# Kernel optimization log

Measured on AMD Instinct MI355X. Metric: run time of the kernel, lower is better.

The kernel has to match this reference:

```python
import jax, jax.numpy as jnp
import numpy as np

B, D_IN, D_HID, D_OUT = 32768, 512, 1024, 2048

def setup_inputs() -> dict:
    key = jax.random.key(0)
    k1, k2, k3, k4 = jax.random.split(key, 4)
    x = jax.random.normal(k1, (B, D_IN), dtype=jnp.float32)
    # linear1 params (torch Linear default-style init, scale approximated)
    l1_w = jax.random.normal(k2, (D_HID, D_IN), dtype=jnp.float32) * (D_IN ** -0.5)
    l1_b = jax.random.normal(k3, (D_HID,), dtype=jnp.float32) * 0.01
    # second linear params: normal(0, hidden^-0.5) weight, zero bias as in source
    weight = jax.random.normal(k4, (D_OUT, D_HID), dtype=jnp.float32) * (D_HID ** -0.5)
    bias = jnp.zeros((D_OUT,), dtype=jnp.float32)
    return {"x": x, "l1_w": l1_w, "l1_b": l1_b, "weight": weight, "bias": bias}

def reference(x, l1_w, l1_b, weight, bias):
    # linear1: [B, D_IN] -> [B, D_HID]
    h = jnp.einsum('bi,hi->bh', x, l1_w) + l1_b
    # fused linear + max epilogue: scores [B, D_OUT] -> max over output dim
    scores = jnp.einsum('bh,oh->bo', h, weight) + bias
    return jnp.max(scores, axis=-1)  # [B]
```

## Files before the change

kernel.cpp:

```cpp
#include <hip/hip_runtime.h>
#include <hip/hip_bf16.h>
#include <stdint.h>

static constexpr int BATCH = 32768;
static constexpr int DIN   = 512;
static constexpr int DHID  = 1024;
static constexpr int DOUT  = 2048;

typedef __bf16 bf16x8 __attribute__((ext_vector_type(8)));
typedef float  f32x4  __attribute__((ext_vector_type(4)));

__device__ __forceinline__ unsigned short f2bf(float f) {
    unsigned int u = __float_as_uint(f);
    u += 0x7FFFu + ((u >> 16) & 1u);
    return (unsigned short)(u >> 16);
}

__device__ __forceinline__ void gload_lds16(const void* g, void* l) {
    __builtin_amdgcn_global_load_lds((__attribute__((address_space(1))) void*)g,
                                     (__attribute__((address_space(3))) void*)l,
                                     16, 0, 0);
}


__global__ __launch_bounds__(256) void prep_kernel(
    const float* __restrict__ w1, const float4* __restrict__ w2f,
    const float4* __restrict__ xf, const float* __restrict__ b1,
    const float* __restrict__ b2,
    unsigned short* __restrict__ w1t, ushort4* __restrict__ w2b,
    ushort4* __restrict__ xb, float* __restrict__ bp) {
    const int blk = blockIdx.x;
    const int t   = threadIdx.x;
    if (blk < 512) {
        __shared__ float tile[32][33];
        const int tileI = blk & 15;
        const int tileH = blk >> 4;
        const int iBase = tileI * 32, hBase = tileH * 32;
        const int col = t & 31, rowq = t >> 5;
#pragma unroll
        for (int p = 0; p < 4; ++p) {
            const int row = p * 8 + rowq;
            tile[row][col] = w1[(size_t)(hBase + row) * DIN + iBase + col];
        }
        __syncthreads();
#pragma unroll
        for (int p = 0; p < 4; ++p) {
            const int row = p * 8 + rowq;
            w1t[(size_t)(iBase + row) * DHID + hBase + col] = f2bf(tile[col][row]);
        }
    } else if (blk < 2560) {
        __shared__ float wsum[4];
        const int o = blk - 512;
        const size_t g = (size_t)o * 256 + t;
        float4 v = w2f[g];
        ushort4 ob;
        ob.x = f2bf(v.x); ob.y = f2bf(v.y); ob.z = f2bf(v.z); ob.w = f2bf(v.w);
        w2b[g] = ob;
        float4 bv = ((const float4*)b1)[t];
        float s = v.x * bv.x + v.y * bv.y + v.z * bv.z + v.w * bv.w;
#pragma unroll
        for (int off = 1; off < 64; off <<= 1) s += __shfl_xor(s, off);
        if ((t & 63) == 0) wsum[t >> 6] = s;
        __syncthreads();
        if (t == 0) bp[o] = wsum[0] + wsum[1] + wsum[2] + wsum[3] + b2[o];
    } else {
        const size_t g = (size_t)(blk - 2560) * 256 + t;
        float4 v = xf[g];
        ushort4 o;
        o.x = f2bf(v.x); o.y = f2bf(v.y); o.z = f2bf(v.z); o.w = f2bf(v.w);
        xb[g] = o;
    }
}

__global__ __launch_bounds__(256) void gemmW_kernel(
    const unsigned short* __restrict__ A,
    const unsigned short* __restrict__ Bw,
    unsigned short* __restrict__ W) {
    constexpr int K = DHID;
    __shared__ __align__(16) unsigned short sA[64 * 128];
    __shared__ __align__(16) unsigned short sB[64 * 128];

    const int tid  = threadIdx.x;
    const int lane = tid & 63;
    const int wid  = tid >> 6;
    const int wr = wid >> 1, wc = wid & 1;
    const int r = lane & 15, q = lane >> 4;
    const int blockN = blockIdx.x * 64;
    const int blockM = blockIdx.y * 64;

    const int chKey = (tid & 15) ^ ((tid >> 4) & 15);
    const size_t aBase = (size_t)(blockM + (tid >> 4)) * K + chKey * 8;
    const size_t bBase = (size_t)(blockN + (tid >> 4)) * K + chKey * 8;

    f32x4 acc[2][2];
#pragma unroll
    for (int mt = 0; mt < 2; ++mt)
#pragma unroll
        for (int nt = 0; nt < 2; ++nt) { f32x4 z = {0.f, 0.f, 0.f, 0.f}; acc[mt][nt] = z; }

    for (int k0 = 0; k0 < K; k0 += 128) {
#pragma unroll
        for (int j = 0; j < 4; ++j) {
            gload_lds16(A  + aBase + (size_t)j * 16 * K + k0, sA + j * 2048 + wid * 512);
            gload_lds16(Bw + bBase + (size_t)j * 16 * K + k0, sB + j * 2048 + wid * 512);
        }
        __syncthreads();
#pragma unroll
        for (int ks = 0; ks < 4; ++ks) {
            const int ch = ((ks << 2) + q) ^ r;
            bf16x8 af[2], bf[2];
#pragma unroll
            for (int mt = 0; mt < 2; ++mt) af[mt] = *(const bf16x8*)&sA[(wr * 32 + mt * 16 + r) * 128 + ch * 8];
#pragma unroll
            for (int nt = 0; nt < 2; ++nt) bf[nt] = *(const bf16x8*)&sB[(wc * 32 + nt * 16 + r) * 128 + ch * 8];
#pragma unroll
            for (int mt = 0; mt < 2; ++mt)
#pragma unroll
                for (int nt = 0; nt < 2; ++nt)
                    acc[mt][nt] = __builtin_amdgcn_mfma_f32_16x16x32_bf16(af[mt], bf[nt], acc[mt][nt], 0, 0, 0);
        }
        __syncthreads();
    }

#pragma unroll
    for (int mt = 0; mt < 2; ++mt) {
        const int row0 = blockM + wr * 32 + mt * 16 + q * 4;
#pragma unroll
        for (int nt = 0; nt < 2; ++nt) {
            const int col = blockN + wc * 32 + nt * 16 + r;
#pragma unroll
            for (int reg = 0; reg < 4; ++reg)
                W[(size_t)(row0 + reg) * DIN + col] = f2bf(acc[mt][nt][reg]);
        }
    }
}

__global__ __launch_bounds__(512, 2) void gemmS_kernel(
    const unsigned short* __restrict__ A,
    const unsigned short* __restrict__ Bw,
    const float* __restrict__ bp,
    float* __restrict__ partials) {
    constexpr int K = DIN;
    __shared__ __align__(16) unsigned short lds[65536];

    const int tid  = threadIdx.x;
    const int lane = tid & 63;
    const int wid  = tid >> 6;
    const int wr   = wid >> 2;
    const int wc   = wid & 3;
    const int r    = lane & 15, q = lane >> 4;

    const int g    = blockIdx.x;
    const int xcd  = g & 7;
    const int i    = g >> 3;
    const int mIdx = xcd * 16 + (i >> 3);
    const int nIdx = i & 7;
    const int blockM = mIdx * 256;
    const int blockN = nIdx * 256;

    const int sRow = tid >> 2;
    const int swz  = (tid & 3) ^ ((tid >> 3) & 3);
    const unsigned short* aSrc = A  + (size_t)(blockM + sRow) * K + swz * 8;
    const unsigned short* bSrc = Bw + (size_t)(blockN + sRow) * K + swz * 8;
    unsigned short* ldsW = lds + wid * 512;

#define STAGE(srcPtr, isB, buf, kh, kt) do {                                    \
    gload_lds16((srcPtr) + (kt) * 64 + (kh) * 32,                               \
                ldsW + (buf) * 32768 + (isB) * 16384 + (kh) * 8192);            \
    gload_lds16((srcPtr) + 128 * K + (kt) * 64 + (kh) * 32,                     \
                ldsW + (buf) * 32768 + (isB) * 16384 + (kh) * 8192 + 4096);     \
} while (0)

    const int rsw  = (r >> 1) & 3;
    const int fOff = (q ^ rsw) * 8;
    const unsigned short* ldsAf = lds + (wr * 128 + r) * 32 + fOff;
    const unsigned short* ldsBf = lds + 16384 + (wc * 64 + r) * 32 + fOff;

    f32x4 acc[8][4];
#pragma unroll
    for (int mt = 0; mt < 8; ++mt)
#pragma unroll
        for (int nt = 0; nt < 4; ++nt) { f32x4 z = {0.f, 0.f, 0.f, 0.f}; acc[mt][nt] = z; }
    bf16x8 af[4], bfr[4];

#define LDA(buf, ks, mg) do {                                                   \
    const unsigned short* p_ = ldsAf + (buf) * 32768 + (ks) * 8192 + (mg) * 2048; \
    af[0] = *(const bf16x8*)(p_);                                               \
    af[1] = *(const bf16x8*)(p_ + 512);                                         \
    af[2] = *(const bf16x8*)(p_ + 1024);                                        \
    af[3] = *(const bf16x8*)(p_ + 1536);                                        \
} while (0)
#define LDB(buf, ks) do {                                                       \
    const unsigned short* p_ = ldsBf + (buf) * 32768 + (ks) * 8192;             \
    bfr[0] = *(const bf16x8*)(p_);                                              \
    bfr[1] = *(const bf16x8*)(p_ + 512);                                        \
    bfr[2] = *(const bf16x8*)(p_ + 1024);                                       \
    bfr[3] = *(const bf16x8*)(p_ + 1536);                                       \
} while (0)
#define MM(mg) do {                                                             \
    __builtin_amdgcn_s_setprio(1);                                              \
    _Pragma("unroll") for (int m_ = 0; m_ < 4; ++m_)                            \
    _Pragma("unroll") for (int n_ = 0; n_ < 4; ++n_)                            \
        acc[(mg) * 4 + m_][n_] = __builtin_amdgcn_mfma_f32_16x16x32_bf16(       \
            af[m_], bfr[n_], acc[(mg) * 4 + m_][n_], 0, 0, 0);                  \
    __builtin_amdgcn_s_setprio(0);                                              \
} while (0)
#define BAR()   __builtin_amdgcn_s_barrier()
#define LGKM0() asm volatile("s_waitcnt lgkmcnt(0)" ::: "memory")
#define VMC(n)  asm volatile("s_waitcnt vmcnt(" #n ")" ::: "memory")

    STAGE(bSrc, 1, 0, 0, 0);
    STAGE(aSrc, 0, 0, 0, 0);
    STAGE(bSrc, 1, 0, 1, 0);
    STAGE(aSrc, 0, 0, 1, 0);
    STAGE(bSrc, 1, 1, 0, 1);
    STAGE(aSrc, 0, 1, 0, 1);
    STAGE(bSrc, 1, 1, 1, 1);
    VMC(6);
    BAR();

#pragma unroll 1
    for (int it = 0; it < 3; ++it) {
        const int t1 = 2 * it + 1, n0 = 2 * it + 2, n1 = 2 * it + 3;
        LDA(0, 0, 0); LDB(0, 0); STAGE(aSrc, 0, 1, 1, t1);
        BAR(); LGKM0(); MM(0); BAR();
        LDA(0, 0, 1); STAGE(bSrc, 1, 0, 0, n0);
        BAR(); LGKM0(); MM(1); BAR();
        LDA(0, 1, 0); LDB(0, 1); STAGE(aSrc, 0, 0, 0, n0);
        BAR(); LGKM0(); MM(0); BAR();
        LDA(0, 1, 1); STAGE(bSrc, 1, 0, 1, n0); VMC(6);
        BAR(); LGKM0(); MM(1); BAR();
        LDA(1, 0, 0); LDB(1, 0); STAGE(aSrc, 0, 0, 1, n0);
        BAR(); LGKM0(); MM(0); BAR();
        LDA(1, 0, 1); STAGE(bSrc, 1, 1, 0, n1);
        BAR(); LGKM0(); MM(1); BAR();
        LDA(1, 1, 0); LDB(1, 1); STAGE(aSrc, 0, 1, 0, n1);
        BAR(); LGKM0(); MM(0); BAR();
        LDA(1, 1, 1); STAGE(bSrc, 1, 1, 1, n1); VMC(6);
        BAR(); LGKM0(); MM(1); BAR();
    }
    LDA(0, 0, 0); LDB(0, 0); STAGE(aSrc, 0, 1, 1, 7);
    BAR(); LGKM0(); MM(0); BAR();
    LDA(0, 0, 1);
    BAR(); LGKM0(); MM(1); BAR();
    LDA(0, 1, 0); LDB(0, 1);
    BAR(); LGKM0(); MM(0); BAR();
    LDA(0, 1, 1); VMC(0);
    BAR(); LGKM0(); MM(1); BAR();
    LDA(1, 0, 0); LDB(1, 0);
    BAR(); LGKM0(); MM(0); BAR();
    LDA(1, 0, 1);
    BAR(); LGKM0(); MM(1); BAR();
    LDA(1, 1, 0); LDB(1, 1);
    BAR(); LGKM0(); MM(0); BAR();
    LDA(1, 1, 1);
    BAR(); LGKM0(); MM(1);

#undef STAGE
#undef LDA
#undef LDB
#undef MM
#undef BAR
#undef LGKM0
#undef VMC

    const int colBase = blockN + wc * 64;
    float bv[4];
#pragma unroll
    for (int nt = 0; nt < 4; ++nt) bv[nt] = bp[colBase + nt * 16 + r];

#pragma unroll
    for (int mt = 0; mt < 8; ++mt) {
#pragma unroll
        for (int reg = 0; reg < 4; ++reg) {
            float v = fmaxf(fmaxf(acc[mt][0][reg] + bv[0], acc[mt][1][reg] + bv[1]),
                            fmaxf(acc[mt][2][reg] + bv[2], acc[mt][3][reg] + bv[3]));
#pragma unroll
            for (int off = 1; off < 16; off <<= 1)
                v = fmaxf(v, __shfl_xor(v, off));
            if (r == 0) {
                const int row = blockM + wr * 128 + mt * 16 + q * 4 + reg;
                partials[(size_t)row * 32 + nIdx * 4 + wc] = v;
            }
        }
    }
}

__global__ __launch_bounds__(256) void reduce_kernel(
    const float4* __restrict__ partials, float* __restrict__ out) {
    const int row = blockIdx.x * blockDim.x + threadIdx.x;
    const float4* p = partials + (size_t)row * 8;
    float m = -INFINITY;
#pragma unroll
    for (int i = 0; i < 8; ++i) {
        float4 v = p[i];
        m = fmaxf(m, fmaxf(fmaxf(v.x, v.y), fmaxf(v.z, v.w)));
    }
    out[row] = m;
}

extern "C" void kernel_launch(void* const* d_in, const int* in_sizes, int n_in,
                              void* d_out, int out_size, void* d_ws, size_t ws_size,
                              hipStream_t stream) {
    const float* x   = (const float*)d_in[0];
    const float* l1w = (const float*)d_in[1];
    const float* l1b = (const float*)d_in[2];
    const float* w2  = (const float*)d_in[3];
    const float* b2  = (const float*)d_in[4];
    float* out = (float*)d_out;

    char* ws = (char*)d_ws;
    unsigned short* w1t = (unsigned short*)(ws);
    unsigned short* w2b = (unsigned short*)(ws + 1048576);
    unsigned short* Wb  = (unsigned short*)(ws + 5242880);
    float* bp           = (float*)(ws + 7340032);
    unsigned short* xb  = (unsigned short*)(ws + 7348224);
    float* partials     = (float*)(ws + 40902656);

    prep_kernel<<<18944, 256, 0, stream>>>(
        l1w, (const float4*)w2, (const float4*)x, l1b, b2,
        w1t, (ushort4*)w2b, (ushort4*)xb, bp);

    gemmW_kernel<<<dim3(DIN / 64, DOUT / 64), 256, 0, stream>>>(w2b, w1t, Wb);

    gemmS_kernel<<<1024, 512, 0, stream>>>(xb, Wb, bp, partials);

    reduce_kernel<<<BATCH / 256, 256, 0, stream>>>((const float4*)partials, out);
}
```

Measured before the change: 192.7 us.

## Make gemmS persistent over four M tiles, prefetching next tile during K tail

The score GEMM now launches 256 blocks instead of 1024. Each block walks four consecutive 256-row M tiles for a fixed N tile. The next tile's first A/B K-slices are staged into LDS during the current tile's last K steps, which removes the per-block prologue and drain bubbles. The B tile stays hot across tiles. In exchange there are fewer blocks than two per CU on a 256-CU part, and the epilogue max-reduction now runs serially between tiles, where it can stall the pipeline.

```diff
diff --git a/kernel.cpp b/kernel.cpp
--- a/kernel.cpp
+++ b/kernel.cpp
@@ -150,18 +150,18 @@
     const int wc   = wid & 3;
     const int r    = lane & 15, q = lane >> 4;
 
-    const int g    = blockIdx.x;
-    const int xcd  = g & 7;
-    const int i    = g >> 3;
-    const int mIdx = xcd * 16 + (i >> 3);
-    const int nIdx = i & 7;
-    const int blockM = mIdx * 256;
-    const int blockN = nIdx * 256;
+    const int b    = blockIdx.x;
+    const int xcd  = b & 7;
+    const int j    = b >> 3;
+    const int nIdx = j & 7;
+    const int mGrp = xcd * 4 + (j >> 3);
+    const int blockM0 = mGrp * 4 * 256;
+    const int blockN  = nIdx * 256;
 
     const int sRow = tid >> 2;
     const int swz  = (tid & 3) ^ ((tid >> 3) & 3);
-    const unsigned short* aSrc = A  + (size_t)(blockM + sRow) * K + swz * 8;
-    const unsigned short* bSrc = Bw + (size_t)(blockN + sRow) * K + swz * 8;
+    const unsigned short* aCur = A  + (size_t)(blockM0 + sRow) * K + swz * 8;
+    const unsigned short* bSrc = Bw + (size_t)(blockN  + sRow) * K + swz * 8;
     unsigned short* ldsW = lds + wid * 512;
 
 #define STAGE(srcPtr, isB, buf, kh, kt) do {                                    \
@@ -209,52 +209,110 @@
 #define LGKM0() asm volatile("s_waitcnt lgkmcnt(0)" ::: "memory")
 #define VMC(n)  asm volatile("s_waitcnt vmcnt(" #n ")" ::: "memory")
 
+#define EPILOG(tt) do {                                                         \
+    const int rowB_ = blockM0 + (tt) * 256 + wr * 128;                          \
+    _Pragma("unroll") for (int mt_ = 0; mt_ < 8; ++mt_) {                       \
+        _Pragma("unroll") for (int rg_ = 0; rg_ < 4; ++rg_) {                   \
+            float v_ = fmaxf(fmaxf(acc[mt_][0][rg_] + bv[0],                    \
+                                   acc[mt_][1][rg_] + bv[1]),                   \
+                             fmaxf(acc[mt_][2][rg_] + bv[2],                    \
+                                   acc[mt_][3][rg_] + bv[3]));                  \
+            _Pragma("unroll") for (int of_ = 1; of_ < 16; of_ <<= 1)            \
+                v_ = fmaxf(v_, __shfl_xor(v_, of_));                            \
+            if (r == 0) {                                                       \
+                const int row_ = rowB_ + mt_ * 16 + q * 4 + rg_;                \
+                partials[(size_t)row_ * 32 + nIdx * 4 + wc] = v_;               \
+            }                                                                   \
+        }                                                                       \
+    }                                                                           \
+} while (0)
+
+#define ACC_ZERO() do {                                                         \
+    _Pragma("unroll") for (int mt_ = 0; mt_ < 8; ++mt_)                         \
+    _Pragma("unroll") for (int nt_ = 0; nt_ < 4; ++nt_) {                       \
+        f32x4 z_ = {0.f, 0.f, 0.f, 0.f}; acc[mt_][nt_] = z_;                    \
+    }                                                                           \
+} while (0)
+
+    const int colBase = blockN + wc * 64;
+    float bv[4];
+#pragma unroll
+    for (int nt = 0; nt < 4; ++nt) bv[nt] = bp[colBase + nt * 16 + r];
+    VMC(0);
+
     STAGE(bSrc, 1, 0, 0, 0);
-    STAGE(aSrc, 0, 0, 0, 0);
+    STAGE(aCur, 0, 0, 0, 0);
     STAGE(bSrc, 1, 0, 1, 0);
-    STAGE(aSrc, 0, 0, 1, 0);
+    STAGE(aCur, 0, 0, 1, 0);
     STAGE(bSrc, 1, 1, 0, 1);
-    STAGE(aSrc, 0, 1, 0, 1);
+    STAGE(aCur, 0, 1, 0, 1);
     STAGE(bSrc, 1, 1, 1, 1);
     VMC(6);
     BAR();
 
 #pragma unroll 1
-    for (int it = 0; it < 3; ++it) {
-        const int t1 = 2 * it + 1, n0 = 2 * it + 2, n1 = 2 * it + 3;
-        LDA(0, 0, 0); LDB(0, 0); STAGE(aSrc, 0, 1, 1, t1);
-        BAR(); LGKM0(); MM(0); BAR();
-        LDA(0, 0, 1); STAGE(bSrc, 1, 0, 0, n0);
-        BAR(); LGKM0(); MM(1); BAR();
-        LDA(0, 1, 0); LDB(0, 1); STAGE(aSrc, 0, 0, 0, n0);
-        BAR(); LGKM0(); MM(0); BAR();
-        LDA(0, 1, 1); STAGE(bSrc, 1, 0, 1, n0); VMC(6);
-        BAR(); LGKM0(); MM(1); BAR();
-        LDA(1, 0, 0); LDB(1, 0); STAGE(aSrc, 0, 0, 1, n0);
-        BAR(); LGKM0(); MM(0); BAR();
-        LDA(1, 0, 1); STAGE(bSrc, 1, 1, 0, n1);
-        BAR(); LGKM0(); MM(1); BAR();
-        LDA(1, 1, 0); LDB(1, 1); STAGE(aSrc, 0, 1, 0, n1);
-        BAR(); LGKM0(); MM(0); BAR();
-        LDA(1, 1, 1); STAGE(bSrc, 1, 1, 1, n1); VMC(6);
-        BAR(); LGKM0(); MM(1); BAR();
-    }
-    LDA(0, 0, 0); LDB(0, 0); STAGE(aSrc, 0, 1, 1, 7);
-    BAR(); LGKM0(); MM(0); BAR();
-    LDA(0, 0, 1);
-    BAR(); LGKM0(); MM(1); BAR();
-    LDA(0, 1, 0); LDB(0, 1);
-    BAR(); LGKM0(); MM(0); BAR();
-    LDA(0, 1, 1); VMC(0);
-    BAR(); LGKM0(); MM(1); BAR();
-    LDA(1, 0, 0); LDB(1, 0);
-    BAR(); LGKM0(); MM(0); BAR();
-    LDA(1, 0, 1);
-    BAR(); LGKM0(); MM(1); BAR();
-    LDA(1, 1, 0); LDB(1, 1);
-    BAR(); LGKM0(); MM(0); BAR();
-    LDA(1, 1, 1);
-    BAR(); LGKM0(); MM(1);
+    for (int t = 0; t < 4; ++t) {
+#pragma unroll 1
+        for (int i2 = 0; i2 < 3; ++i2) {
+            const int k1 = 2 * i2 + 1, k2 = 2 * i2 + 2, k3 = 2 * i2 + 3;
+            LDA(0, 0, 0); LDB(0, 0); STAGE(aCur, 0, 1, 1, k1);
+            BAR(); LGKM0(); MM(0); BAR();
+            LDA(0, 0, 1); STAGE(bSrc, 1, 0, 0, k2);
+            BAR(); LGKM0(); MM(1); BAR();
+            LDA(0, 1, 0); LDB(0, 1); STAGE(aCur, 0, 0, 0, k2);
+            BAR(); LGKM0(); MM(0); BAR();
+            LDA(0, 1, 1); STAGE(bSrc, 1, 0, 1, k2); VMC(6);
+            BAR(); LGKM0(); MM(1); BAR();
+            LDA(1, 0, 0); LDB(1, 0); STAGE(aCur, 0, 0, 1, k2);
+            BAR(); LGKM0(); MM(0); BAR();
+            LDA(1, 0, 1); STAGE(bSrc, 1, 1, 0, k3);
+            BAR(); LGKM0(); MM(1); BAR();
+            LDA(1, 1, 0); LDB(1, 1); STAGE(aCur, 0, 1, 0, k3);
+            BAR(); LGKM0(); MM(0); BAR();
+            LDA(1, 1, 1); STAGE(bSrc, 1, 1, 1, k3); VMC(6);
+            BAR(); LGKM0(); MM(1); BAR();
+        }
+        if (t < 3) {
+            const unsigned short* aNxt = aCur + 256 * K;
+            LDA(0, 0, 0); LDB(0, 0); STAGE(aCur, 0, 1, 1, 7);
+            BAR(); LGKM0(); MM(0); BAR();
+            LDA(0, 0, 1); STAGE(bSrc, 1, 0, 0, 0);
+            BAR(); LGKM0(); MM(1); BAR();
+            LDA(0, 1, 0); LDB(0, 1); STAGE(aNxt, 0, 0, 0, 0);
+            BAR(); LGKM0(); MM(0); BAR();
+            LDA(0, 1, 1); STAGE(bSrc, 1, 0, 1, 0); VMC(6);
+            BAR(); LGKM0(); MM(1); BAR();
+            LDA(1, 0, 0); LDB(1, 0); STAGE(aNxt, 0, 0, 1, 0);
+            BAR(); LGKM0(); MM(0); BAR();
+            LDA(1, 0, 1); STAGE(bSrc, 1, 1, 0, 1);
+            BAR(); LGKM0(); MM(1); BAR();
+            LDA(1, 1, 0); LDB(1, 1); STAGE(aNxt, 0, 1, 0, 1);
+            BAR(); LGKM0(); MM(0); BAR();
+            LDA(1, 1, 1); STAGE(bSrc, 1, 1, 1, 1); VMC(6);
+            BAR(); LGKM0(); MM(1); BAR();
+            EPILOG(t);
+            ACC_ZERO();
+            aCur = aNxt;
+        } else {
+            LDA(0, 0, 0); LDB(0, 0); STAGE(aCur, 0, 1, 1, 7);
+            BAR(); LGKM0(); MM(0); BAR();
+            LDA(0, 0, 1);
+            BAR(); LGKM0(); MM(1); BAR();
+            LDA(0, 1, 0); LDB(0, 1);
+            BAR(); LGKM0(); MM(0); BAR();
+            LDA(0, 1, 1); VMC(0);
+            BAR(); LGKM0(); MM(1); BAR();
+            LDA(1, 0, 0); LDB(1, 0);
+            BAR(); LGKM0(); MM(0); BAR();
+            LDA(1, 0, 1);
+            BAR(); LGKM0(); MM(1); BAR();
+            LDA(1, 1, 0); LDB(1, 1);
+            BAR(); LGKM0(); MM(0); BAR();
+            LDA(1, 1, 1);
+            BAR(); LGKM0(); MM(1);
+            EPILOG(3);
+        }
+    }
 
 #undef STAGE
 #undef LDA
@@ -263,27 +321,8 @@
 #undef BAR
 #undef LGKM0
 #undef VMC
-
-    const int colBase = blockN + wc * 64;
-    float bv[4];
-#pragma unroll
-    for (int nt = 0; nt < 4; ++nt) bv[nt] = bp[colBase + nt * 16 + r];
-
-#pragma unroll
-    for (int mt = 0; mt < 8; ++mt) {
-#pragma unroll
-        for (int reg = 0; reg < 4; ++reg) {
-            float v = fmaxf(fmaxf(acc[mt][0][reg] + bv[0], acc[mt][1][reg] + bv[1]),
-                            fmaxf(acc[mt][2][reg] + bv[2], acc[mt][3][reg] + bv[3]));
-#pragma unroll
-            for (int off = 1; off < 16; off <<= 1)
-                v = fmaxf(v, __shfl_xor(v, off));
-            if (r == 0) {
-                const int row = blockM + wr * 128 + mt * 16 + q * 4 + reg;
-                partials[(size_t)row * 32 + nIdx * 4 + wc] = v;
-            }
-        }
-    }
+#undef EPILOG
+#undef ACC_ZERO
 }
 
 __global__ __launch_bounds__(256) void reduce_kernel(
@@ -323,7 +362,7 @@
 
     gemmW_kernel<<<dim3(DIN / 64, DOUT / 64), 256, 0, stream>>>(w2b, w1t, Wb);
 
-    gemmS_kernel<<<1024, 512, 0, stream>>>(xb, Wb, bp, partials);
+    gemmS_kernel<<<256, 512, 0, stream>>>(xb, Wb, bp, partials);
 
     reduce_kernel<<<BATCH / 256, 256, 0, stream>>>((const float4*)partials, out);
 }
```

Result: slower. 357.3 us (+85.4%).

## Loop each gemmS block over four N tiles with running max accumulation

Applied to the files above, without the earlier changes.

The scores GEMM now launches 256 blocks instead of 1024. Each block owns one 256-row M tile and walks four consecutive 256-column N tiles, prefetching the next B tile during the tail of the current one. After each tile it folds the bias-added accumulators into a per-thread running max held in registers, then zeroes them. This cuts the partials footprint fourfold and simplifies the reduce kernel, but 256 blocks may underfill the GPU's CUs and the extra mx registers may raise register pressure.

```diff
diff --git a/kernel.cpp b/kernel.cpp
--- a/kernel.cpp
+++ b/kernel.cpp
@@ -141,7 +141,7 @@
     const float* __restrict__ bp,
     float* __restrict__ partials) {
     constexpr int K = DIN;
-    __shared__ __align__(16) unsigned short lds[65536];
+    __shared__ __align__(16) unsigned short lds[67584];
 
     const int tid  = threadIdx.x;
     const int lane = tid & 63;
@@ -150,19 +150,20 @@
     const int wc   = wid & 3;
     const int r    = lane & 15, q = lane >> 4;
 
-    const int g    = blockIdx.x;
-    const int xcd  = g & 7;
-    const int i    = g >> 3;
-    const int mIdx = xcd * 16 + (i >> 3);
-    const int nIdx = i & 7;
-    const int blockM = mIdx * 256;
-    const int blockN = nIdx * 256;
+    const int b    = blockIdx.x;
+    const int xcd  = b & 7;
+    const int j    = b >> 3;
+    const int nGrp = j & 1;
+    const int mIdx = xcd * 16 + (j >> 1);
+    const int blockM  = mIdx * 256;
+    const int blockN0 = nGrp * 1024;
 
     const int sRow = tid >> 2;
     const int swz  = (tid & 3) ^ ((tid >> 3) & 3);
-    const unsigned short* aSrc = A  + (size_t)(blockM + sRow) * K + swz * 8;
-    const unsigned short* bSrc = Bw + (size_t)(blockN + sRow) * K + swz * 8;
+    const unsigned short* aSrc = A  + (size_t)(blockM  + sRow) * K + swz * 8;
+    const unsigned short* bCur = Bw + (size_t)(blockN0 + sRow) * K + swz * 8;
     unsigned short* ldsW = lds + wid * 512;
+    float* biasLds = (float*)(lds + 65536);
 
 #define STAGE(srcPtr, isB, buf, kh, kt) do {                                    \
     gload_lds16((srcPtr) + (kt) * 64 + (kh) * 32,                               \
@@ -181,7 +182,13 @@
     for (int mt = 0; mt < 8; ++mt)
 #pragma unroll
         for (int nt = 0; nt < 4; ++nt) { f32x4 z = {0.f, 0.f, 0.f, 0.f}; acc[mt][nt] = z; }
+    float mx[8][4];
+#pragma unroll
+    for (int mt = 0; mt < 8; ++mt)
+#pragma unroll
+        for (int rg = 0; rg < 4; ++rg) mx[mt][rg] = -INFINITY;
     bf16x8 af[4], bfr[4];
+    float bvc[4];
 
 #define LDA(buf, ks, mg) do {                                                   \
     const unsigned short* p_ = ldsAf + (buf) * 32768 + (ks) * 8192 + (mg) * 2048; \
@@ -209,52 +216,109 @@
 #define LGKM0() asm volatile("s_waitcnt lgkmcnt(0)" ::: "memory")
 #define VMC(n)  asm volatile("s_waitcnt vmcnt(" #n ")" ::: "memory")
 
-    STAGE(bSrc, 1, 0, 0, 0);
+#define FOLD() do {                                                             \
+    _Pragma("unroll") for (int mt_ = 0; mt_ < 8; ++mt_)                         \
+    _Pragma("unroll") for (int rg_ = 0; rg_ < 4; ++rg_) {                       \
+        float v_ = fmaxf(fmaxf(acc[mt_][0][rg_] + bvc[0],                       \
+                               acc[mt_][1][rg_] + bvc[1]),                      \
+                         fmaxf(acc[mt_][2][rg_] + bvc[2],                       \
+                               acc[mt_][3][rg_] + bvc[3]));                     \
+        mx[mt_][rg_] = fmaxf(mx[mt_][rg_], v_);                                 \
+    }                                                                           \
+} while (0)
+
+#define ACC_ZERO() do {                                                         \
+    _Pragma("unroll") for (int mt_ = 0; mt_ < 8; ++mt_)                         \
+    _Pragma("unroll") for (int nt_ = 0; nt_ < 4; ++nt_) {                       \
+        f32x4 z_ = {0.f, 0.f, 0.f, 0.f}; acc[mt_][nt_] = z_;                    \
+    }                                                                           \
+} while (0)
+
+    {
+        float2 bb = ((const float2*)(bp + blockN0))[tid];
+        ((float2*)biasLds)[tid] = bb;
+    }
+    LGKM0();
+
+    STAGE(bCur, 1, 0, 0, 0);
     STAGE(aSrc, 0, 0, 0, 0);
-    STAGE(bSrc, 1, 0, 1, 0);
+    STAGE(bCur, 1, 0, 1, 0);
     STAGE(aSrc, 0, 0, 1, 0);
-    STAGE(bSrc, 1, 1, 0, 1);
+    STAGE(bCur, 1, 1, 0, 1);
     STAGE(aSrc, 0, 1, 0, 1);
-    STAGE(bSrc, 1, 1, 1, 1);
+    STAGE(bCur, 1, 1, 1, 1);
     VMC(6);
     BAR();
 
+#pragma unroll
+    for (int nt = 0; nt < 4; ++nt) bvc[nt] = biasLds[wc * 64 + nt * 16 + r];
+
 #pragma unroll 1
-    for (int it = 0; it < 3; ++it) {
-        const int t1 = 2 * it + 1, n0 = 2 * it + 2, n1 = 2 * it + 3;
-        LDA(0, 0, 0); LDB(0, 0); STAGE(aSrc, 0, 1, 1, t1);
-        BAR(); LGKM0(); MM(0); BAR();
-        LDA(0, 0, 1); STAGE(bSrc, 1, 0, 0, n0);
-        BAR(); LGKM0(); MM(1); BAR();
-        LDA(0, 1, 0); LDB(0, 1); STAGE(aSrc, 0, 0, 0, n0);
-        BAR(); LGKM0(); MM(0); BAR();
-        LDA(0, 1, 1); STAGE(bSrc, 1, 0, 1, n0); VMC(6);
-        BAR(); LGKM0(); MM(1); BAR();
-        LDA(1, 0, 0); LDB(1, 0); STAGE(aSrc, 0, 0, 1, n0);
-        BAR(); LGKM0(); MM(0); BAR();
-        LDA(1, 0, 1); STAGE(bSrc, 1, 1, 0, n1);
-        BAR(); LGKM0(); MM(1); BAR();
-        LDA(1, 1, 0); LDB(1, 1); STAGE(aSrc, 0, 1, 0, n1);
-        BAR(); LGKM0(); MM(0); BAR();
-        LDA(1, 1, 1); STAGE(bSrc, 1, 1, 1, n1); VMC(6);
-        BAR(); LGKM0(); MM(1); BAR();
-    }
-    LDA(0, 0, 0); LDB(0, 0); STAGE(aSrc, 0, 1, 1, 7);
-    BAR(); LGKM0(); MM(0); BAR();
-    LDA(0, 0, 1);
-    BAR(); LGKM0(); MM(1); BAR();
-    LDA(0, 1, 0); LDB(0, 1);
-    BAR(); LGKM0(); MM(0); BAR();
-    LDA(0, 1, 1); VMC(0);
-    BAR(); LGKM0(); MM(1); BAR();
-    LDA(1, 0, 0); LDB(1, 0);
-    BAR(); LGKM0(); MM(0); BAR();
-    LDA(1, 0, 1);
-    BAR(); LGKM0(); MM(1); BAR();
-    LDA(1, 1, 0); LDB(1, 1);
-    BAR(); LGKM0(); MM(0); BAR();
-    LDA(1, 1, 1);
-    BAR(); LGKM0(); MM(1);
+    for (int t = 0; t < 4; ++t) {
+#pragma unroll 1
+        for (int i2 = 0; i2 < 3; ++i2) {
+            const int k1 = 2 * i2 + 1, k2 = 2 * i2 + 2, k3 = 2 * i2 + 3;
+            LDA(0, 0, 0); LDB(0, 0); STAGE(aSrc, 0, 1, 1, k1);
+            BAR(); LGKM0(); MM(0); BAR();
+            LDA(0, 0, 1); STAGE(bCur, 1, 0, 0, k2);
+            BAR(); LGKM0(); MM(1); BAR();
+            LDA(0, 1, 0); LDB(0, 1); STAGE(aSrc, 0, 0, 0, k2);
+            BAR(); LGKM0(); MM(0); BAR();
+            LDA(0, 1, 1); STAGE(bCur, 1, 0, 1, k2); VMC(6);
+            BAR(); LGKM0(); MM(1); BAR();
+            LDA(1, 0, 0); LDB(1, 0); STAGE(aSrc, 0, 0, 1, k2);
+            BAR(); LGKM0(); MM(0); BAR();
+            LDA(1, 0, 1); STAGE(bCur, 1, 1, 0, k3);
+            BAR(); LGKM0(); MM(1); BAR();
+            LDA(1, 1, 0); LDB(1, 1); STAGE(aSrc, 0, 1, 0, k3);
+            BAR(); LGKM0(); MM(0); BAR();
+            LDA(1, 1, 1); STAGE(bCur, 1, 1, 1, k3); VMC(6);
+            BAR(); LGKM0(); MM(1); BAR();
+        }
+        if (t < 3) {
+            const unsigned short* bNxt = bCur + 256 * K;
+            LDA(0, 0, 0); LDB(0, 0); STAGE(aSrc, 0, 1, 1, 7);
+            BAR(); LGKM0(); MM(0); BAR();
+            LDA(0, 0, 1); STAGE(bNxt, 1, 0, 0, 0);
+            BAR(); LGKM0(); MM(1); BAR();
+            LDA(0, 1, 0); LDB(0, 1); STAGE(aSrc, 0, 0, 0, 0);
+            BAR(); LGKM0(); MM(0); BAR();
+            LDA(0, 1, 1); STAGE(bNxt, 1, 0, 1, 0); VMC(6);
+            BAR(); LGKM0(); MM(1); BAR();
+            LDA(1, 0, 0); LDB(1, 0); STAGE(aSrc, 0, 0, 1, 0);
+            BAR(); LGKM0(); MM(0); BAR();
+            LDA(1, 0, 1); STAGE(bNxt, 1, 1, 0, 1);
+            BAR(); LGKM0(); MM(1); BAR();
+            LDA(1, 1, 0); LDB(1, 1); STAGE(aSrc, 0, 1, 0, 1);
+            BAR(); LGKM0(); MM(0); BAR();
+            LDA(1, 1, 1); STAGE(bNxt, 1, 1, 1, 1); VMC(6);
+            BAR(); LGKM0(); MM(1); BAR();
+            FOLD();
+            ACC_ZERO();
+#pragma unroll
+            for (int nt = 0; nt < 4; ++nt)
+                bvc[nt] = biasLds[(t + 1) * 256 + wc * 64 + nt * 16 + r];
+            bCur = bNxt;
+        } else {
+            LDA(0, 0, 0); LDB(0, 0); STAGE(aSrc, 0, 1, 1, 7);
+            BAR(); LGKM0(); MM(0); BAR();
+            LDA(0, 0, 1);
+            BAR(); LGKM0(); MM(1); BAR();
+            LDA(0, 1, 0); LDB(0, 1);
+            BAR(); LGKM0(); MM(0); BAR();
+            LDA(0, 1, 1); VMC(0);
+            BAR(); LGKM0(); MM(1); BAR();
+            LDA(1, 0, 0); LDB(1, 0);
+            BAR(); LGKM0(); MM(0); BAR();
+            LDA(1, 0, 1);
+            BAR(); LGKM0(); MM(1); BAR();
+            LDA(1, 1, 0); LDB(1, 1);
+            BAR(); LGKM0(); MM(0); BAR();
+            LDA(1, 1, 1);
+            BAR(); LGKM0(); MM(1);
+            FOLD();
+        }
+    }
 
 #undef STAGE
 #undef LDA
@@ -263,24 +327,20 @@
 #undef BAR
 #undef LGKM0
 #undef VMC
-
-    const int colBase = blockN + wc * 64;
-    float bv[4];
-#pragma unroll
-    for (int nt = 0; nt < 4; ++nt) bv[nt] = bp[colBase + nt * 16 + r];
+#undef FOLD
+#undef ACC_ZERO
 
 #pragma unroll
     for (int mt = 0; mt < 8; ++mt) {
 #pragma unroll
-        for (int reg = 0; reg < 4; ++reg) {
-            float v = fmaxf(fmaxf(acc[mt][0][reg] + bv[0], acc[mt][1][reg] + bv[1]),
-                            fmaxf(acc[mt][2][reg] + bv[2], acc[mt][3][reg] + bv[3]));
+        for (int rg = 0; rg < 4; ++rg) {
+            float v = mx[mt][rg];
 #pragma unroll
             for (int off = 1; off < 16; off <<= 1)
                 v = fmaxf(v, __shfl_xor(v, off));
             if (r == 0) {
-                const int row = blockM + wr * 128 + mt * 16 + q * 4 + reg;
-                partials[(size_t)row * 32 + nIdx * 4 + wc] = v;
+                const int row = blockM + wr * 128 + mt * 16 + q * 4 + rg;
+                partials[(size_t)row * 8 + nGrp * 4 + wc] = v;
             }
         }
     }
@@ -289,13 +349,10 @@
 __global__ __launch_bounds__(256) void reduce_kernel(
     const float4* __restrict__ partials, float* __restrict__ out) {
     const int row = blockIdx.x * blockDim.x + threadIdx.x;
-    const float4* p = partials + (size_t)row * 8;
-    float m = -INFINITY;
-#pragma unroll
-    for (int i = 0; i < 8; ++i) {
-        float4 v = p[i];
-        m = fmaxf(m, fmaxf(fmaxf(v.x, v.y), fmaxf(v.z, v.w)));
-    }
+    const float4* p = partials + (size_t)row * 2;
+    float4 v0 = p[0], v1 = p[1];
+    float m = fmaxf(fmaxf(fmaxf(v0.x, v0.y), fmaxf(v0.z, v0.w)),
+                    fmaxf(fmaxf(v1.x, v1.y), fmaxf(v1.z, v1.w)));
     out[row] = m;
 }
 
@@ -323,7 +380,7 @@
 
     gemmW_kernel<<<dim3(DIN / 64, DOUT / 64), 256, 0, stream>>>(w2b, w1t, Wb);
 
-    gemmS_kernel<<<1024, 512, 0, stream>>>(xb, Wb, bp, partials);
+    gemmS_kernel<<<256, 512, 0, stream>>>(xb, Wb, bp, partials);
 
     reduce_kernel<<<BATCH / 256, 256, 0, stream>>>((const float4*)partials, out);
 }
```

Measured after the change: 382.7 us. +98.6%, slower.
